# Performance work log

Hardware: AMD Instinct MI355X
Metric: run time of the kernel (lower is better)

## Reference

```python
import jax, jax.numpy as jnp
import numpy as np

P = 4096        # n_particles
D = 64          # embedding_dim
H = 4           # attention heads
HD = D // H     # head dim
N = 1_000_000   # n_collisions


def setup_inputs() -> dict:
    key = jax.random.key(0)
    ks = jax.random.split(key, 24)
    s = lambda k, shape, fan: jax.random.normal(k, shape, jnp.float32) / np.sqrt(fan)
    inp = {
        'times': jax.random.normal(ks[0], (N,), jnp.float32),
        'momentum_transfers': jax.random.normal(ks[1], (N,), jnp.float32),
        'positions': jax.random.normal(ks[2], (N,), jnp.float32),
        'particle_pairs': jax.random.randint(ks[3], (N, 2), 0, P),
        # event encoder: Linear(3, D)
        'W_enc': s(ks[4], (3, D), 3), 'b_enc': jnp.zeros((D,), jnp.float32),
        # learned particle embeddings
        'pemb': s(ks[5], (P, D), D),
        # MultiheadAttention projections (math layout: y = x @ W + b)
        'Wq': s(ks[6], (D, D), D), 'bq': jnp.zeros((D,), jnp.float32),
        'Wk': s(ks[7], (D, D), D), 'bk': jnp.zeros((D,), jnp.float32),
        'Wv': s(ks[8], (D, D), D), 'bv': jnp.zeros((D,), jnp.float32),
        'Wo': s(ks[9], (D, D), D), 'bo': jnp.zeros((D,), jnp.float32),
        # mass head: Linear(D, D//2) -> ReLU -> Linear(D//2, 1) -> Softplus
        'Wm1': s(ks[10], (D, D // 2), D), 'bm1': jnp.zeros((D // 2,), jnp.float32),
        'Wm2': s(ks[11], (D // 2, 1), D // 2), 'bm2': jnp.zeros((1,), jnp.float32),
        # diameter head
        'Wd1': s(ks[12], (D, D // 2), D), 'bd1': jnp.zeros((D // 2,), jnp.float32),
        'Wd2': s(ks[13], (D // 2, 1), D // 2), 'bd2': jnp.zeros((1,), jnp.float32),
    }
    return inp


def _forward(times, momentum_transfers, positions, particle_pairs,
             W_enc, b_enc, pemb, Wq, bq, Wk, bk, Wv, bv, Wo, bo,
             Wm1, bm1, Wm2, bm2, Wd1, bd1, Wd2, bd2):
    # 1. embed collision events: (N,3) -> (N,D), tanh
    feats = jnp.stack([times, momentum_transfers, positions], axis=-1)
    emb = jnp.tanh(feats @ W_enc + b_enc)  # (N, D)

    # 2. segment-mean pooling into particle bins (both endpoints of each pair)
    idx = particle_pairs.reshape(-1)                     # (2N,)
    vals = jnp.repeat(emb, 2, axis=0)                    # (2N, D) [p1,p2 per event]
    updates = jax.ops.segment_sum(vals, idx, num_segments=P)          # (P, D)
    counts = jax.ops.segment_sum(jnp.ones_like(idx, jnp.float32), idx,
                                 num_segments=P)                      # (P,)
    counts = jnp.clip(counts, 1.0)
    x = pemb + updates / counts[:, None]                 # (P, D)

    # 3. self-attention over particles (batch of 1)
    q = (x @ Wq + bq).reshape(P, H, HD)
    k = (x @ Wk + bk).reshape(P, H, HD)
    v = (x @ Wv + bv).reshape(P, H, HD)
    scale = 1.0 / np.sqrt(HD)
    scores = jnp.einsum('phd,qhd->hpq', q * scale, k)    # (H, P, P)
    attn = jax.nn.softmax(scores, axis=-1)
    ctx = jnp.einsum('hpq,qhd->phd', attn, v).reshape(P, D)
    x = ctx @ Wo + bo                                    # (P, D)

    # 4. prediction heads
    masses = jax.nn.softplus(
        (jax.nn.relu(x @ Wm1 + bm1) @ Wm2 + bm2)).squeeze(-1)  # (P,)
    diameters = jax.nn.softplus(
        (jax.nn.relu(x @ Wd1 + bd1) @ Wd2 + bd2)).squeeze(-1)  # (P,)
    return masses, diameters


def reference(times, momentum_transfers, positions, particle_pairs,
              W_enc, b_enc, pemb, Wq, bq, Wk, bk, Wv, bv, Wo, bo,
              Wm1, bm1, Wm2, bm2, Wd1, bd1, Wd2, bd2):
    return _forward(times, momentum_transfers, positions, particle_pairs,
                    W_enc, b_enc, pemb, Wq, bq, Wk, bk, Wv, bv, Wo, bo,
                    Wm1, bm1, Wm2, bm2, Wd1, bd1, Wd2, bd2)
```

## Files before the change

kernel.cpp:

```cpp
#include <hip/hip_runtime.h>
#include <hip/hip_fp16.h>
#include <math.h>

#define NP 1000000
#define NE (2 * NP)
#define P 4096
#define D 64
#define H 4
#define HD 16

#define NB 512
#define PBT 1024
#define SCB 128

#define KC 8

typedef short s4v __attribute__((ext_vector_type(4)));
typedef short s8v __attribute__((ext_vector_type(8)));
typedef float f4v __attribute__((ext_vector_type(4)));

__device__ __forceinline__ float softplus_f(float x) {
    return fmaxf(x, 0.0f) + log1pf(__expf(-fabsf(x)));
}
__device__ __forceinline__ unsigned short f2bf_rne(float f) {
    unsigned int b = __float_as_uint(f);
    b += 0x7fffu + ((b >> 16) & 1u);
    return (unsigned short)(b >> 16);
}

__global__ void __launch_bounds__(PBT) hist_pass(const int* __restrict__ pairs,
                                                 int* __restrict__ hists) {
    __shared__ int lh[P];
    const int tid = threadIdx.x, blk = blockIdx.x;
    for (int i = tid; i < P; i += PBT) lh[i] = 0;
    __syncthreads();
    const int lo = (int)(((long long)blk * NE) / NB);
    const int hi = (int)(((long long)(blk + 1) * NE) / NB);
    for (int i = lo + tid; i < hi; i += PBT) atomicAdd(&lh[pairs[i]], 1);
    __syncthreads();
    for (int i = tid; i < P; i += PBT) hists[(size_t)blk * P + i] = lh[i];
}

__global__ void __launch_bounds__(1024) scan_cols(int* __restrict__ hists,
                                                  int* __restrict__ totals) {
    __shared__ int buf[64][SCB];
    const int bo = blockIdx.x * SCB;
    const int t = threadIdx.x;
    const int col = t & (SCB - 1);
    const int row = t >> 7;
    int carry = 0;
    for (int c = 0; c < NB / 64; ++c) {
#pragma unroll
        for (int r8 = 0; r8 < 64; r8 += 8)
            buf[r8 + row][col] = hists[(size_t)(c * 64 + r8 + row) * P + bo + col];
        __syncthreads();
        if (t < SCB) {
            int cr = carry;
            for (int r = 0; r < 64; ++r) { int v = buf[r][t]; buf[r][t] = cr; cr += v; }
            carry = cr;
        }
        __syncthreads();
#pragma unroll
        for (int r8 = 0; r8 < 64; r8 += 8)
            hists[(size_t)(c * 64 + r8 + row) * P + bo + col] = buf[r8 + row][col];
        __syncthreads();
    }
    if (t < SCB) totals[bo + t] = carry;
}

__global__ void __launch_bounds__(1024) scan_bins(const int* __restrict__ totals,
                                                  int* __restrict__ bin_start) {
    __shared__ int sdat[1024];
    const int t = threadIdx.x;
    int a[4]; int s = 0;
#pragma unroll
    for (int k2 = 0; k2 < 4; ++k2) { a[k2] = totals[t * 4 + k2]; s += a[k2]; }
    sdat[t] = s;
    __syncthreads();
    for (int off = 1; off < 1024; off <<= 1) {
        int v = (t >= off) ? sdat[t - off] : 0;
        __syncthreads();
        sdat[t] += v;
        __syncthreads();
    }
    int run = sdat[t] - s;
#pragma unroll
    for (int k2 = 0; k2 < 4; ++k2) { bin_start[t * 4 + k2] = run; run += a[k2]; }
    if (t == 1023) bin_start[P] = run;
}

__global__ void __launch_bounds__(PBT) place_pass(
        const int* __restrict__ pairs, const float* __restrict__ times,
        const float* __restrict__ mom, const float* __restrict__ pos,
        const int* __restrict__ hists, const int* __restrict__ bin_start,
        uint2* __restrict__ sfeats) {
    __shared__ int lc[P];
    __shared__ int loff[P];
    const int tid = threadIdx.x, blk = blockIdx.x;
    for (int i = tid; i < P; i += PBT) {
        lc[i] = 0;
        loff[i] = bin_start[i] + hists[(size_t)blk * P + i];
    }
    __syncthreads();
    const int lo = (int)(((long long)blk * NE) / NB);
    const int hi = (int)(((long long)(blk + 1) * NE) / NB);
    int idx[4]; bool vld[4]; int bb[4]; uint2 ff[4];
#pragma unroll
    for (int j = 0; j < 4; ++j) {
        idx[j] = lo + tid + j * PBT;
        vld[j] = idx[j] < hi;
        int i2 = vld[j] ? idx[j] : lo;
        int ev = i2 >> 1;
        bb[j] = pairs[i2];
        __half2 tm = __floats2half2_rn(times[ev], mom[ev]);
        __half2 pz = __floats2half2_rn(pos[ev], 0.0f);
        ff[j].x = *(unsigned int*)&tm;
        ff[j].y = *(unsigned int*)&pz;
    }
    int rr[4];
#pragma unroll
    for (int j = 0; j < 4; ++j)
        rr[j] = vld[j] ? atomicAdd(&lc[bb[j]], 1) : 0;
#pragma unroll
    for (int j = 0; j < 4; ++j)
        if (vld[j]) sfeats[(size_t)loff[bb[j]] + rr[j]] = ff[j];
}

#define GBODY(fx, fy, fz)                                                      \
    {                                                                          \
        float u0 = fmaf(fx, w0a[0], fmaf(fy, w1a[0], fmaf(fz, w2a[0], ba[0]))); \
        float u1 = fmaf(fx, w0a[1], fmaf(fy, w1a[1], fmaf(fz, w2a[1], ba[1]))); \
        float u2 = fmaf(fx, w0a[2], fmaf(fy, w1a[2], fmaf(fz, w2a[2], ba[2]))); \
        float u3 = fmaf(fx, w0a[3], fmaf(fy, w1a[3], fmaf(fz, w2a[3], ba[3]))); \
        float u4 = fmaf(fx, w0b[0], fmaf(fy, w1b[0], fmaf(fz, w2b[0], bbv[0]))); \
        float u5 = fmaf(fx, w0b[1], fmaf(fy, w1b[1], fmaf(fz, w2b[1], bbv[1]))); \
        float u6 = fmaf(fx, w0b[2], fmaf(fy, w1b[2], fmaf(fz, w2b[2], bbv[2]))); \
        float u7 = fmaf(fx, w0b[3], fmaf(fy, w1b[3], fmaf(fz, w2b[3], bbv[3]))); \
        racc[0] += __builtin_amdgcn_rcpf(__builtin_amdgcn_exp2f(u0) + 1.0f);   \
        racc[1] += __builtin_amdgcn_rcpf(__builtin_amdgcn_exp2f(u1) + 1.0f);   \
        racc[2] += __builtin_amdgcn_rcpf(__builtin_amdgcn_exp2f(u2) + 1.0f);   \
        racc[3] += __builtin_amdgcn_rcpf(__builtin_amdgcn_exp2f(u3) + 1.0f);   \
        racc[4] += __builtin_amdgcn_rcpf(__builtin_amdgcn_exp2f(u4) + 1.0f);   \
        racc[5] += __builtin_amdgcn_rcpf(__builtin_amdgcn_exp2f(u5) + 1.0f);   \
        racc[6] += __builtin_amdgcn_rcpf(__builtin_amdgcn_exp2f(u6) + 1.0f);   \
        racc[7] += __builtin_amdgcn_rcpf(__builtin_amdgcn_exp2f(u7) + 1.0f);   \
    }

#define UNPACK(u, fx, fy, fz)                                                  \
    float fx, fy, fz;                                                          \
    {                                                                          \
        float2 t2 = __half22float2(*(__half2*)&(u).x);                         \
        fx = t2.x; fy = t2.y;                                                  \
        fz = __half2float(*(__half*)&(u).y);                                   \
    }

__global__ void __launch_bounds__(512) gather_kernel(
        const uint2* __restrict__ sfeats, const int* __restrict__ bin_start,
        const float* __restrict__ Wenc, const float* __restrict__ benc,
        const float* __restrict__ pemb, float* __restrict__ x) {
    __shared__ float sred[4][16][68];
    const int tid = threadIdx.x;
    const int wv = tid >> 6, ln = tid & 63;
    const int bi = wv >> 1, hw = wv & 1;
    const int es = ln & 7, dg = ln >> 3;
    const int b = blockIdx.x * 4 + bi;
    const int d0 = dg * 8;
    const float C = 2.8853900817779268f;
    f4v w0a = *(const f4v*)(Wenc + d0);          f4v w0b = *(const f4v*)(Wenc + d0 + 4);
    f4v w1a = *(const f4v*)(Wenc + D + d0);      f4v w1b = *(const f4v*)(Wenc + D + d0 + 4);
    f4v w2a = *(const f4v*)(Wenc + 2 * D + d0);  f4v w2b = *(const f4v*)(Wenc + 2 * D + d0 + 4);
    f4v ba  = *(const f4v*)(benc + d0);          f4v bbv = *(const f4v*)(benc + d0 + 4);
    w0a *= C; w0b *= C; w1a *= C; w1b *= C; w2a *= C; w2b *= C; ba *= C; bbv *= C;

    const int s0 = bin_start[b], s1 = bin_start[b + 1];
    const int cnt = s1 - s0;
    const int half = (cnt + 1) >> 1;
    const int lo = s0 + hw * half;
    const int hi = hw ? s1 : (s0 + half);

    float racc[8];
#pragma unroll
    for (int j = 0; j < 8; ++j) racc[j] = 0.0f;
    int ncnt = 0;
    int base = lo;
    for (; base + 16 <= hi; base += 16) {
        uint2 u0 = sfeats[base + es];
        uint2 u1 = sfeats[base + 8 + es];
        { UNPACK(u0, fx0, fy0, fz0); GBODY(fx0, fy0, fz0); }
        { UNPACK(u1, fx1, fy1, fz1); GBODY(fx1, fy1, fz1); }
        ncnt += 2;
    }
    if (base + 8 <= hi) {
        uint2 u0 = sfeats[base + es];
        { UNPACK(u0, fx0, fy0, fz0); GBODY(fx0, fy0, fz0); }
        ncnt += 1;
        base += 8;
    }
    if (base < hi) {
        const int n = hi - base;
        const bool valid = es < n;
        uint2 u0 = valid ? sfeats[base + es] : make_uint2(0u, 0u);
        float save[8];
#pragma unroll
        for (int j = 0; j < 8; ++j) save[j] = racc[j];
        { UNPACK(u0, fx0, fy0, fz0); GBODY(fx0, fy0, fz0); }
        if (!valid) {
#pragma unroll
            for (int j = 0; j < 8; ++j) racc[j] = save[j];
        } else {
            ncnt += 1;
        }
    }
    const float fn = (float)ncnt;
    float* sw = &sred[bi][hw * 8 + es][d0];
#pragma unroll
    for (int j = 0; j < 8; ++j) sw[j] = fmaf(-2.0f, racc[j], fn);
    __syncthreads();
    if (tid < 256) {
        int bin = tid >> 6, dim = tid & 63;
        float s = 0.0f;
#pragma unroll
        for (int e2 = 0; e2 < 16; ++e2) s += sred[bin][e2][dim];
        int gb = blockIdx.x * 4 + bin;
        float c2 = (float)(bin_start[gb + 1] - bin_start[gb]);
        x[gb * D + dim] = pemb[gb * D + dim] + s / fmaxf(c2, 1.0f);
    }
}

__global__ void qkv_kernel(const float* __restrict__ x,
                           const float* __restrict__ Wq, const float* __restrict__ bq,
                           const float* __restrict__ Wk, const float* __restrict__ bk,
                           const float* __restrict__ Wv, const float* __restrict__ bv,
                           unsigned short* __restrict__ Qb, unsigned short* __restrict__ Kf,
                           unsigned short* __restrict__ Vf) {
    __shared__ float xs[4][D];
    const int r0 = blockIdx.x * 4;
    const int tid = threadIdx.x;
    xs[tid >> 6][tid & 63] = x[r0 * D + tid];
    __syncthreads();
    const int row = tid >> 6, col = tid & 63;
    float aq = bq[col], ak = bk[col], av = bv[col];
    for (int d = 0; d < D; ++d) {
        float xv = xs[row][d];
        aq = fmaf(xv, Wq[d * D + col], aq);
        ak = fmaf(xv, Wk[d * D + col], ak);
        av = fmaf(xv, Wv[d * D + col], av);
    }
    const int h = col >> 4, hd = col & 15, gr = r0 + row;
    Qb[((h * P + gr) << 4) + hd] = f2bf_rne(aq * 0.3606737602222409f);
    const int kb = gr >> 5, kk = gr & 31, up = kk >> 4;
    Kf[(((size_t)h * 128 + kb) * 64 + (hd >> 2) * 16 + (kk & 15)) * 8 + up * 4 + (hd & 3)] =
        f2bf_rne(ak);
    Vf[(((size_t)h * 128 + kb) * 64 + ((kk & 15) >> 2) * 16 + hd) * 8 + up * 4 + (kk & 3)] =
        f2bf_rne(av);
}

__global__ void __launch_bounds__(256) flash_kernel(
        const unsigned short* __restrict__ Qb, const unsigned short* __restrict__ Kf,
        const unsigned short* __restrict__ Vf,
        float* __restrict__ pl, float* __restrict__ pout) {
    const int bid = blockIdx.x;
    const int h  = bid & 3;
    const int qt = (bid >> 2) & 63;
    const int kc = bid >> 8;
    const int tid = threadIdx.x;
    const int wv = tid >> 6, lane = tid & 63;
    const int g = lane >> 4, li = lane & 15;
    const int q0 = qt * 64 + wv * 16;

    s8v qf = {0, 0, 0, 0, 0, 0, 0, 0};
    {
        s4v ql = *(const s4v*)(Qb + ((size_t)(h * P + q0 + li) << 4) + 4 * g);
        qf[0] = ql[0]; qf[1] = ql[1]; qf[2] = ql[2]; qf[3] = ql[3];
    }
    const unsigned short* Kh = Kf + (size_t)h * 128 * 512;
    const unsigned short* Vh = Vf + (size_t)h * 128 * 512;

    f4v accA = {0.f, 0.f, 0.f, 0.f};
    f4v accB = {0.f, 0.f, 0.f, 0.f};
    float lA = 0.f, lB = 0.f;
    const int kb0 = kc * (P / KC / 32);
    const int kb1 = kb0 + P / KC / 32;
#pragma unroll 4
    for (int kb = kb0; kb < kb1; kb += 2) {
        s8v kf1 = *(const s8v*)(Kh + ((size_t)kb * 64 + lane) * 8);
        s8v kf2 = *(const s8v*)(Kh + ((size_t)(kb + 1) * 64 + lane) * 8);
        s8v vf1 = *(const s8v*)(Vh + ((size_t)kb * 64 + lane) * 8);
        s8v vf2 = *(const s8v*)(Vh + ((size_t)(kb + 1) * 64 + lane) * 8);
        s8v ka1 = {kf1[0], kf1[1], kf1[2], kf1[3], 0, 0, 0, 0};
        s8v ka2 = {kf1[4], kf1[5], kf1[6], kf1[7], 0, 0, 0, 0};
        s8v ka3 = {kf2[0], kf2[1], kf2[2], kf2[3], 0, 0, 0, 0};
        s8v ka4 = {kf2[4], kf2[5], kf2[6], kf2[7], 0, 0, 0, 0};
        f4v z = {0.f, 0.f, 0.f, 0.f};
        f4v c1 = __builtin_amdgcn_mfma_f32_16x16x32_bf16(ka1, qf, z, 0, 0, 0);
        f4v c2 = __builtin_amdgcn_mfma_f32_16x16x32_bf16(ka2, qf, z, 0, 0, 0);
        f4v c3 = __builtin_amdgcn_mfma_f32_16x16x32_bf16(ka3, qf, z, 0, 0, 0);
        f4v c4 = __builtin_amdgcn_mfma_f32_16x16x32_bf16(ka4, qf, z, 0, 0, 0);
        float p0 = __builtin_amdgcn_exp2f(c1[0]), p1 = __builtin_amdgcn_exp2f(c1[1]);
        float p2 = __builtin_amdgcn_exp2f(c1[2]), p3 = __builtin_amdgcn_exp2f(c1[3]);
        float p4 = __builtin_amdgcn_exp2f(c2[0]), p5 = __builtin_amdgcn_exp2f(c2[1]);
        float p6 = __builtin_amdgcn_exp2f(c2[2]), p7 = __builtin_amdgcn_exp2f(c2[3]);
        float p8 = __builtin_amdgcn_exp2f(c3[0]), p9 = __builtin_amdgcn_exp2f(c3[1]);
        float pa = __builtin_amdgcn_exp2f(c3[2]), pb = __builtin_amdgcn_exp2f(c3[3]);
        float pc = __builtin_amdgcn_exp2f(c4[0]), pd = __builtin_amdgcn_exp2f(c4[1]);
        float pe = __builtin_amdgcn_exp2f(c4[2]), pf_ = __builtin_amdgcn_exp2f(c4[3]);
        lA += ((p0 + p1) + (p2 + p3)) + ((p4 + p5) + (p6 + p7));
        lB += ((p8 + p9) + (pa + pb)) + ((pc + pd) + (pe + pf_));
        s8v pf1, pf2;
        pf1[0] = (short)(__float_as_uint(p0) >> 16); pf1[1] = (short)(__float_as_uint(p1) >> 16);
        pf1[2] = (short)(__float_as_uint(p2) >> 16); pf1[3] = (short)(__float_as_uint(p3) >> 16);
        pf1[4] = (short)(__float_as_uint(p4) >> 16); pf1[5] = (short)(__float_as_uint(p5) >> 16);
        pf1[6] = (short)(__float_as_uint(p6) >> 16); pf1[7] = (short)(__float_as_uint(p7) >> 16);
        pf2[0] = (short)(__float_as_uint(p8) >> 16); pf2[1] = (short)(__float_as_uint(p9) >> 16);
        pf2[2] = (short)(__float_as_uint(pa) >> 16); pf2[3] = (short)(__float_as_uint(pb) >> 16);
        pf2[4] = (short)(__float_as_uint(pc) >> 16); pf2[5] = (short)(__float_as_uint(pd) >> 16);
        pf2[6] = (short)(__float_as_uint(pe) >> 16); pf2[7] = (short)(__float_as_uint(pf_) >> 16);
        accA = __builtin_amdgcn_mfma_f32_16x16x32_bf16(vf1, pf1, accA, 0, 0, 0);
        accB = __builtin_amdgcn_mfma_f32_16x16x32_bf16(vf2, pf2, accB, 0, 0, 0);
    }
    f4v acc = {accA[0] + accB[0], accA[1] + accB[1], accA[2] + accB[2], accA[3] + accB[3]};
    float l = lA + lB;
    l += __shfl_xor(l, 16, 64);
    l += __shfl_xor(l, 32, 64);
    const int q = q0 + li;
    const size_t gidx = (size_t)(h * P + q) * KC + kc;
    *(f4v*)(pout + gidx * 16 + 4 * g) = acc;
    if (lane < 16) pl[gidx] = l;
}

__global__ void heads_kernel(const float* __restrict__ pl, const float* __restrict__ pout,
                             const float* __restrict__ Wo, const float* __restrict__ bo,
                             const float* __restrict__ Wm1, const float* __restrict__ bm1,
                             const float* __restrict__ Wm2, const float* __restrict__ bm2,
                             const float* __restrict__ Wd1, const float* __restrict__ bd1,
                             const float* __restrict__ Wd2, const float* __restrict__ bd2,
                             float* __restrict__ out) {
    __shared__ float cs[4][D];
    __shared__ float x2[4][D];
    __shared__ float hid[4][D];
    const int r0 = blockIdx.x * 4;
    const int tid = threadIdx.x;
    const int row = tid >> 6, col = tid & 63;
    {
        const int h = col >> 4, hd = col & 15;
        const size_t gq = (size_t)(h * P + r0 + row);
        float L = 0.f, s = 0.f;
#pragma unroll
        for (int c = 0; c < KC; ++c) {
            L += pl[gq * KC + c];
            s += pout[(gq * KC + c) * 16 + hd];
        }
        cs[row][col] = s / L;
    }
    __syncthreads();
    float a = bo[col];
    for (int d = 0; d < D; ++d) a = fmaf(cs[row][d], Wo[d * D + col], a);
    x2[row][col] = a;
    __syncthreads();
    const int hc = col & 31;
    const float* W1 = (col < 32) ? Wm1 : Wd1;
    float hsum = (col < 32) ? bm1[hc] : bd1[hc];
    for (int d = 0; d < D; ++d) hsum = fmaf(x2[row][d], W1[d * 32 + hc], hsum);
    hsum = fmaxf(hsum, 0.0f);
    float w2 = (col < 32) ? Wm2[hc] : Wd2[hc];
    hid[row][col] = hsum * w2;
    __syncthreads();
    if (tid < 8) {
        int rr = tid >> 1, which = tid & 1;
        float s = which ? bd2[0] : bm2[0];
        for (int j2 = 0; j2 < 32; ++j2) s += hid[rr][which * 32 + j2];
        out[which * P + r0 + rr] = softplus_f(s);
    }
}

extern "C" void kernel_launch(void* const* d_in, const int* in_sizes, int n_in,
                              void* d_out, int out_size, void* d_ws, size_t ws_size,
                              hipStream_t stream) {
    const float* times = (const float*)d_in[0];
    const float* mom   = (const float*)d_in[1];
    const float* pos   = (const float*)d_in[2];
    const int*   pairs = (const int*)d_in[3];
    const float* Wenc  = (const float*)d_in[4];
    const float* benc  = (const float*)d_in[5];
    const float* pemb  = (const float*)d_in[6];
    const float* Wq = (const float*)d_in[7];   const float* bq = (const float*)d_in[8];
    const float* Wk = (const float*)d_in[9];   const float* bk = (const float*)d_in[10];
    const float* Wv = (const float*)d_in[11];  const float* bv = (const float*)d_in[12];
    const float* Wo = (const float*)d_in[13];  const float* bo = (const float*)d_in[14];
    const float* Wm1 = (const float*)d_in[15]; const float* bm1 = (const float*)d_in[16];
    const float* Wm2 = (const float*)d_in[17]; const float* bm2 = (const float*)d_in[18];
    const float* Wd1 = (const float*)d_in[19]; const float* bd1 = (const float*)d_in[20];
    const float* Wd2 = (const float*)d_in[21]; const float* bd2 = (const float*)d_in[22];

    char* wsb = (char*)d_ws;
    uint2* sfeats   = (uint2*)wsb;
    int* hists      = (int*)(wsb + (size_t)NE * 8);
    int* totals     = hists + (size_t)NB * P;
    int* bin_start  = totals + P;
    float* x        = (float*)(bin_start + P + 2);
    unsigned short* Qb = (unsigned short*)(x + P * D);
    unsigned short* Kf = Qb + (size_t)H * P * 16;
    unsigned short* Vf = Kf + (size_t)H * P * 16;
    float* pl       = (float*)(Vf + (size_t)H * P * 16);
    float* pout     = (float*)wsb;
    float* out      = (float*)d_out;

    hist_pass<<<NB, PBT, 0, stream>>>(pairs, hists);
    scan_cols<<<P / SCB, 1024, 0, stream>>>(hists, totals);
    scan_bins<<<1, 1024, 0, stream>>>(totals, bin_start);
    place_pass<<<NB, PBT, 0, stream>>>(pairs, times, mom, pos, hists, bin_start, sfeats);
    gather_kernel<<<P / 4, 512, 0, stream>>>(sfeats, bin_start, Wenc, benc, pemb, x);
    qkv_kernel<<<P / 4, 256, 0, stream>>>(x, Wq, bq, Wk, bk, Wv, bv, Qb, Kf, Vf);
    flash_kernel<<<H * (P / 64) * KC, 256, 0, stream>>>(Qb, Kf, Vf, pl, pout);
    heads_kernel<<<P / 4, 256, 0, stream>>>(pl, pout, Wo, bo, Wm1, bm1, Wm2, bm2,
                                            Wd1, bd1, Wd2, bd2, out);
}
```

Measured before the change: 130.8 us.

## Pair reciprocals in gather sigmoid sum and split bins across four waves

```diff
diff --git a/kernel.cpp b/kernel.cpp
--- a/kernel.cpp
+++ b/kernel.cpp
@@ -126,44 +126,49 @@
         if (vld[j]) sfeats[(size_t)loff[bb[j]] + rr[j]] = ff[j];
 }
 
-#define GBODY(fx, fy, fz)                                                      \
+#define PDIM(w0_, w1_, w2_, b_, j)                                             \
     {                                                                          \
-        float u0 = fmaf(fx, w0a[0], fmaf(fy, w1a[0], fmaf(fz, w2a[0], ba[0]))); \
-        float u1 = fmaf(fx, w0a[1], fmaf(fy, w1a[1], fmaf(fz, w2a[1], ba[1]))); \
-        float u2 = fmaf(fx, w0a[2], fmaf(fy, w1a[2], fmaf(fz, w2a[2], ba[2]))); \
-        float u3 = fmaf(fx, w0a[3], fmaf(fy, w1a[3], fmaf(fz, w2a[3], ba[3]))); \
-        float u4 = fmaf(fx, w0b[0], fmaf(fy, w1b[0], fmaf(fz, w2b[0], bbv[0]))); \
-        float u5 = fmaf(fx, w0b[1], fmaf(fy, w1b[1], fmaf(fz, w2b[1], bbv[1]))); \
-        float u6 = fmaf(fx, w0b[2], fmaf(fy, w1b[2], fmaf(fz, w2b[2], bbv[2]))); \
-        float u7 = fmaf(fx, w0b[3], fmaf(fy, w1b[3], fmaf(fz, w2b[3], bbv[3]))); \
-        racc[0] += __builtin_amdgcn_rcpf(__builtin_amdgcn_exp2f(u0) + 1.0f);   \
-        racc[1] += __builtin_amdgcn_rcpf(__builtin_amdgcn_exp2f(u1) + 1.0f);   \
-        racc[2] += __builtin_amdgcn_rcpf(__builtin_amdgcn_exp2f(u2) + 1.0f);   \
-        racc[3] += __builtin_amdgcn_rcpf(__builtin_amdgcn_exp2f(u3) + 1.0f);   \
-        racc[4] += __builtin_amdgcn_rcpf(__builtin_amdgcn_exp2f(u4) + 1.0f);   \
-        racc[5] += __builtin_amdgcn_rcpf(__builtin_amdgcn_exp2f(u5) + 1.0f);   \
-        racc[6] += __builtin_amdgcn_rcpf(__builtin_amdgcn_exp2f(u6) + 1.0f);   \
-        racc[7] += __builtin_amdgcn_rcpf(__builtin_amdgcn_exp2f(u7) + 1.0f);   \
-    }
-
-#define UNPACK(u, fx, fy, fz)                                                  \
-    float fx, fy, fz;                                                          \
+        float uA = fmaf(fAx, w0_, fmaf(fAy, w1_, fmaf(fAz, w2_, b_)));         \
+        float uB = fmaf(fBx, w0_, fmaf(fBy, w1_, fmaf(fBz, w2_, b_)));         \
+        float pA = __builtin_amdgcn_exp2f(uA) + 1.0f;                          \
+        float pB = __builtin_amdgcn_exp2f(uB) + 1.0f;                          \
+        racc[j] = fmaf(pA + pB, __builtin_amdgcn_rcpf(pA * pB), racc[j]);      \
+    }
+#define GBODY2()                                                               \
+    PDIM(w0a[0], w1a[0], w2a[0], ba[0], 0)                                     \
+    PDIM(w0a[1], w1a[1], w2a[1], ba[1], 1)                                     \
+    PDIM(w0a[2], w1a[2], w2a[2], ba[2], 2)                                     \
+    PDIM(w0a[3], w1a[3], w2a[3], ba[3], 3)                                     \
+    PDIM(w0b[0], w1b[0], w2b[0], bbv[0], 4)                                    \
+    PDIM(w0b[1], w1b[1], w2b[1], bbv[1], 5)                                    \
+    PDIM(w0b[2], w1b[2], w2b[2], bbv[2], 6)                                    \
+    PDIM(w0b[3], w1b[3], w2b[3], bbv[3], 7)
+
+#define SDIM(w0_, w1_, w2_, b_, j)                                             \
     {                                                                          \
-        float2 t2 = __half22float2(*(__half2*)&(u).x);                         \
-        fx = t2.x; fy = t2.y;                                                  \
-        fz = __half2float(*(__half*)&(u).y);                                   \
-    }
+        float u = fmaf(fAx, w0_, fmaf(fAy, w1_, fmaf(fAz, w2_, b_)));          \
+        racc[j] += __builtin_amdgcn_rcpf(__builtin_amdgcn_exp2f(u) + 1.0f);    \
+    }
+#define GBODY1()                                                               \
+    SDIM(w0a[0], w1a[0], w2a[0], ba[0], 0)                                     \
+    SDIM(w0a[1], w1a[1], w2a[1], ba[1], 1)                                     \
+    SDIM(w0a[2], w1a[2], w2a[2], ba[2], 2)                                     \
+    SDIM(w0a[3], w1a[3], w2a[3], ba[3], 3)                                     \
+    SDIM(w0b[0], w1b[0], w2b[0], bbv[0], 4)                                    \
+    SDIM(w0b[1], w1b[1], w2b[1], bbv[1], 5)                                    \
+    SDIM(w0b[2], w1b[2], w2b[2], bbv[2], 6)                                    \
+    SDIM(w0b[3], w1b[3], w2b[3], bbv[3], 7)
 
 __global__ void __launch_bounds__(512) gather_kernel(
         const uint2* __restrict__ sfeats, const int* __restrict__ bin_start,
         const float* __restrict__ Wenc, const float* __restrict__ benc,
         const float* __restrict__ pemb, float* __restrict__ x) {
-    __shared__ float sred[4][16][68];
+    __shared__ float sred[2][32][68];
     const int tid = threadIdx.x;
     const int wv = tid >> 6, ln = tid & 63;
-    const int bi = wv >> 1, hw = wv & 1;
+    const int bi = wv >> 2, qh = wv & 3;
     const int es = ln & 7, dg = ln >> 3;
-    const int b = blockIdx.x * 4 + bi;
+    const int b = blockIdx.x * 2 + bi;
     const int d0 = dg * 8;
     const float C = 2.8853900817779268f;
     f4v w0a = *(const f4v*)(Wenc + d0);          f4v w0b = *(const f4v*)(Wenc + d0 + 4);
@@ -174,9 +179,9 @@
 
     const int s0 = bin_start[b], s1 = bin_start[b + 1];
     const int cnt = s1 - s0;
-    const int half = (cnt + 1) >> 1;
-    const int lo = s0 + hw * half;
-    const int hi = hw ? s1 : (s0 + half);
+    const int qs = (cnt + 3) >> 2;
+    const int lo = s0 + qh * qs;
+    const int hi = min(s0 + (qh + 1) * qs, s1);
 
     float racc[8];
 #pragma unroll
@@ -184,26 +189,33 @@
     int ncnt = 0;
     int base = lo;
     for (; base + 16 <= hi; base += 16) {
-        uint2 u0 = sfeats[base + es];
-        uint2 u1 = sfeats[base + 8 + es];
-        { UNPACK(u0, fx0, fy0, fz0); GBODY(fx0, fy0, fz0); }
-        { UNPACK(u1, fx1, fy1, fz1); GBODY(fx1, fy1, fz1); }
+        uint2 uA = sfeats[base + es];
+        uint2 uB = sfeats[base + 8 + es];
+        float2 tA = __half22float2(*(__half2*)&uA.x);
+        float fAx = tA.x, fAy = tA.y, fAz = __half2float(*(__half*)&uA.y);
+        float2 tB = __half22float2(*(__half2*)&uB.x);
+        float fBx = tB.x, fBy = tB.y, fBz = __half2float(*(__half*)&uB.y);
+        GBODY2();
         ncnt += 2;
     }
     if (base + 8 <= hi) {
-        uint2 u0 = sfeats[base + es];
-        { UNPACK(u0, fx0, fy0, fz0); GBODY(fx0, fy0, fz0); }
+        uint2 uA = sfeats[base + es];
+        float2 tA = __half22float2(*(__half2*)&uA.x);
+        float fAx = tA.x, fAy = tA.y, fAz = __half2float(*(__half*)&uA.y);
+        GBODY1();
         ncnt += 1;
         base += 8;
     }
     if (base < hi) {
         const int n = hi - base;
         const bool valid = es < n;
-        uint2 u0 = valid ? sfeats[base + es] : make_uint2(0u, 0u);
+        uint2 uA = valid ? sfeats[base + es] : make_uint2(0u, 0u);
+        float2 tA = __half22float2(*(__half2*)&uA.x);
+        float fAx = tA.x, fAy = tA.y, fAz = __half2float(*(__half*)&uA.y);
         float save[8];
 #pragma unroll
         for (int j = 0; j < 8; ++j) save[j] = racc[j];
-        { UNPACK(u0, fx0, fy0, fz0); GBODY(fx0, fy0, fz0); }
+        GBODY1();
         if (!valid) {
 #pragma unroll
             for (int j = 0; j < 8; ++j) racc[j] = save[j];
@@ -212,16 +224,16 @@
         }
     }
     const float fn = (float)ncnt;
-    float* sw = &sred[bi][hw * 8 + es][d0];
+    float* sw = &sred[bi][qh * 8 + es][d0];
 #pragma unroll
     for (int j = 0; j < 8; ++j) sw[j] = fmaf(-2.0f, racc[j], fn);
     __syncthreads();
-    if (tid < 256) {
+    if (tid < 128) {
         int bin = tid >> 6, dim = tid & 63;
         float s = 0.0f;
 #pragma unroll
-        for (int e2 = 0; e2 < 16; ++e2) s += sred[bin][e2][dim];
-        int gb = blockIdx.x * 4 + bin;
+        for (int e2 = 0; e2 < 32; ++e2) s += sred[bin][e2][dim];
+        int gb = blockIdx.x * 2 + bin;
         float c2 = (float)(bin_start[gb + 1] - bin_start[gb]);
         x[gb * D + dim] = pemb[gb * D + dim] + s / fmaxf(c2, 1.0f);
     }
@@ -409,7 +421,7 @@
     scan_cols<<<P / SCB, 1024, 0, stream>>>(hists, totals);
     scan_bins<<<1, 1024, 0, stream>>>(totals, bin_start);
     place_pass<<<NB, PBT, 0, stream>>>(pairs, times, mom, pos, hists, bin_start, sfeats);
-    gather_kernel<<<P / 4, 512, 0, stream>>>(sfeats, bin_start, Wenc, benc, pemb, x);
+    gather_kernel<<<P / 2, 512, 0, stream>>>(sfeats, bin_start, Wenc, benc, pemb, x);
     qkv_kernel<<<P / 4, 256, 0, stream>>>(x, Wq, bq, Wk, bk, Wv, bv, Qb, Kf, Vf);
     flash_kernel<<<H * (P / 64) * KC, 256, 0, stream>>>(Qb, Kf, Vf, pl, pout);
     heads_kernel<<<P / 4, 256, 0, stream>>>(pl, pout, Wo, bo, Wm1, bm1, Wm2, bm2,
```

Result: faster. 127.7 us (-2.4%).
